# Kernel optimization log

Hardware: AMD Instinct MI355X
Metric: run time of the kernel (lower is better)

The kernel has to match this reference:

```python
import jax, jax.numpy as jnp
import numpy as np

DEPTH_SCALES = 4  # matches init_kwargs
REDUCTION = 16    # CBAM-style MLP reduction ratio


def setup_inputs() -> dict:
    key = jax.random.key(0)
    k0, k1, k2 = jax.random.split(key, 3)
    N, C, H, W = 32, 512, 64, 64
    D, r = DEPTH_SCALES, REDUCTION
    x = jax.random.normal(k0, (N, C, H, W), dtype=jnp.float32)
    # shared 2-layer gate MLP: C -> C//r -> C*D
    W1 = jax.random.normal(k1, (C, C // r), dtype=jnp.float32) * 0.05
    b1 = jnp.zeros((C // r,), dtype=jnp.float32)
    W2 = jax.random.normal(k2, (C // r, C * D), dtype=jnp.float32) * 0.05
    b2 = jnp.zeros((C * D,), dtype=jnp.float32)
    return {"x": x, "W1": W1, "b1": b1, "W2": W2, "b2": b2}


def reference(x, W1, b1, W2, b2):
    N, C, H, W = x.shape
    D = DEPTH_SCALES
    block = C // D  # block_size

    # ExpandedChannelGate (CBAM-style): avg+max spatial pooling through a
    # shared MLP, summed, sigmoid -> attention [N, C, D]
    avg_pool = jnp.mean(x, axis=(2, 3))  # [N, C]
    max_pool = jnp.max(x, axis=(2, 3))   # [N, C]

    def mlp(p):
        return jax.nn.relu(p @ W1 + b1) @ W2 + b2  # [N, C*D]

    attn = jax.nn.sigmoid(mlp(avg_pool) + mlp(max_pool))  # [N, C*D]
    attn = attn.reshape(N, C, D).transpose(0, 2, 1)       # [N, D, C]

    # topk over the channel axis per (sample, scale); lax.top_k sorts
    # descending like torch.topk
    _, idx = jax.lax.top_k(attn, block)  # [N, D, block]

    # Original concatenates scale-i selections along channel dim, i.e.
    # channel order = [scale0 topk..., scale1 topk..., ...].
    idx_flat = idx.reshape(N, D * block)  # [N, C]

    # single vectorized gather replaces the nested index_select loops
    out = jax.vmap(lambda xi, ii: xi[ii])(x, idx_flat)  # [N, D*block, H, W]
    return out
```

## Files before the change

### kernel.cpp

```cpp
#include <hip/hip_runtime.h>
#include <hip/hip_bf16.h>
#include <math.h>

#define N_ 32
#define C_ 512
#define HW_ 4096
#define D_ 4
#define RHID_ 32
#define BLOCK_ 128
#define C2_ 2048

__global__ __launch_bounds__(256) void pool_kernel(
    const float* __restrict__ x, float* __restrict__ avg_out,
    float* __restrict__ max_out) {
  const int b = blockIdx.x;
  const float4* src = (const float4*)(x + (size_t)b * HW_);
  const int t = threadIdx.x;

  double dsum = 0.0;
  float mx = -INFINITY;
#pragma unroll
  for (int i = 0; i < 4; ++i) {
    float4 v = src[t + i * 256];
    dsum += (double)v.x + (double)v.y + (double)v.z + (double)v.w;
    mx = fmaxf(mx, fmaxf(fmaxf(v.x, v.y), fmaxf(v.z, v.w)));
  }
#pragma unroll
  for (int off = 32; off > 0; off >>= 1) {
    dsum += __shfl_down(dsum, off);
    mx = fmaxf(mx, __shfl_down(mx, off));
  }
  __shared__ double s_sum[4];
  __shared__ float s_max[4];
  const int wave = t >> 6;
  if ((t & 63) == 0) { s_sum[wave] = dsum; s_max[wave] = mx; }
  __syncthreads();
  if (t == 0) {
    double tot = s_sum[0] + s_sum[1] + s_sum[2] + s_sum[3];
    float m = fmaxf(fmaxf(s_max[0], s_max[1]), fmaxf(s_max[2], s_max[3]));
    avg_out[b] = (float)(tot * (1.0 / (double)HW_));
    max_out[b] = m;
  }
}

__global__ __launch_bounds__(256) void mlp_topk_kernel(
    const float* __restrict__ avg, const float* __restrict__ mx,
    const float* __restrict__ W1, const float* __restrict__ b1,
    const float* __restrict__ W2, const float* __restrict__ b2,
    int* __restrict__ idx_out) {
  const int n = blockIdx.x >> 2;
  const int d = blockIdx.x & 3;
  const int t = threadIdx.x;

  __shared__ float s_avg[C_];
  __shared__ float s_mx[C_];
  __shared__ double s_h[RHID_];
  __shared__ unsigned long long s_key[C_];

#pragma unroll
  for (int i = 0; i < 2; ++i) {
    int c = t + i * 256;
    s_avg[c] = avg[n * C_ + c];
    s_mx[c] = mx[n * C_ + c];
  }
  __syncthreads();

  if (t < RHID_) {
    double acc_a = (double)b1[t];
    double acc_m = acc_a;
    for (int c = 0; c < C_; ++c) {
      double w = (double)W1[c * RHID_ + t];
      acc_a += (double)s_avg[c] * w;
      acc_m += (double)s_mx[c] * w;
    }
    s_h[t] = (acc_a > 0.0 ? acc_a : 0.0) + (acc_m > 0.0 ? acc_m : 0.0);
  }
  __syncthreads();

  for (int c = t; c < C_; c += 256) {
    const int col = c * D_ + d;
    double acc = 2.0 * (double)b2[col];
#pragma unroll
    for (int j = 0; j < RHID_; ++j)
      acc += s_h[j] * (double)W2[j * C2_ + col];
    float f = (float)acc;
    unsigned u = __float_as_uint(f);
    u = (u & 0x80000000u) ? ~u : (u | 0x80000000u);
    s_key[c] = ((unsigned long long)u << 32) | (unsigned)(C_ - 1 - c);
  }
  __syncthreads();

  for (int kk = 2; kk <= C_; kk <<= 1) {
    for (int jj = kk >> 1; jj > 0; jj >>= 1) {
#pragma unroll
      for (int r = 0; r < 2; ++r) {
        int i = t + r * 256;
        int ixj = i ^ jj;
        if (ixj > i) {
          bool ddd = ((i & kk) != 0);
          unsigned long long a = s_key[i], b = s_key[ixj];
          if ((a > b) == ddd) { s_key[i] = b; s_key[ixj] = a; }
        }
      }
      __syncthreads();
    }
  }

  if (t < BLOCK_) {
    int c = (C_ - 1) - (int)(s_key[t] & 0xFFFFFFFFu);
    idx_out[(n * D_ + d) * BLOCK_ + t] = c;
  }
}

__global__ __launch_bounds__(256) void gather_kernel(
    const float* __restrict__ x, const int* __restrict__ idx,
    float* __restrict__ out) {
  const int b = blockIdx.x;
  const int n = b >> 9;
  const int c = idx[b];
  const float4* src = (const float4*)(x + ((size_t)(n * C_ + c)) * HW_);
  float4* dst = (float4*)(out + (size_t)b * HW_);
  const int t = threadIdx.x;
#pragma unroll
  for (int i = 0; i < 4; ++i) dst[t + i * 256] = src[t + i * 256];
}

extern "C" void kernel_launch(void* const* d_in, const int* in_sizes, int n_in,
                              void* d_out, int out_size, void* d_ws, size_t ws_size,
                              hipStream_t stream) {
  const float* x  = (const float*)d_in[0];
  const float* W1 = (const float*)d_in[1];
  const float* b1 = (const float*)d_in[2];
  const float* W2 = (const float*)d_in[3];
  const float* b2 = (const float*)d_in[4];
  float* out = (float*)d_out;

  float* ws_avg = (float*)d_ws;
  float* ws_max = ws_avg + N_ * C_;
  int* ws_idx = (int*)(ws_max + N_ * C_);

  pool_kernel<<<N_ * C_, 256, 0, stream>>>(x, ws_avg, ws_max);
  mlp_topk_kernel<<<N_ * D_, 256, 0, stream>>>(ws_avg, ws_max, W1, b1, W2, b2,
                                               ws_idx);
  gather_kernel<<<N_ * C_, 256, 0, stream>>>(x, ws_idx, out);
}
```

Measured before the change: 544.7 us.

## Assign one wavefront per channel in pool/gather and parallelize first MLP layer

Pool and gather kernels now map each 64-lane wavefront to one channel plane, with four planes per block. This drops the shared-memory cross-wave reduction and __syncthreads in pooling, and gives each thread more loads in flight. The gather uses nontemporal stores so the written output does not evict x from cache. The first MLP layer is split across all 256 threads into 8 partial sums reduced in shared memory, replacing a 32-thread serial loop over 512 channels.

```diff
diff --git a/kernel.cpp b/kernel.cpp
--- a/kernel.cpp
+++ b/kernel.cpp
@@ -1,5 +1,4 @@
 #include <hip/hip_runtime.h>
-#include <hip/hip_bf16.h>
 #include <math.h>
 
 #define N_ 32
@@ -10,18 +9,20 @@
 #define BLOCK_ 128
 #define C2_ 2048
 
+typedef float vfloat4 __attribute__((ext_vector_type(4)));
+
 __global__ __launch_bounds__(256) void pool_kernel(
     const float* __restrict__ x, float* __restrict__ avg_out,
     float* __restrict__ max_out) {
-  const int b = blockIdx.x;
-  const float4* src = (const float4*)(x + (size_t)b * HW_);
-  const int t = threadIdx.x;
+  const int p = (blockIdx.x << 2) + (threadIdx.x >> 6);
+  const int lane = threadIdx.x & 63;
+  const vfloat4* src = (const vfloat4*)(x + (size_t)p * HW_);
 
   double dsum = 0.0;
   float mx = -INFINITY;
 #pragma unroll
-  for (int i = 0; i < 4; ++i) {
-    float4 v = src[t + i * 256];
+  for (int i = 0; i < 16; ++i) {
+    vfloat4 v = src[lane + (i << 6)];
     dsum += (double)v.x + (double)v.y + (double)v.z + (double)v.w;
     mx = fmaxf(mx, fmaxf(fmaxf(v.x, v.y), fmaxf(v.z, v.w)));
   }
@@ -30,16 +31,9 @@
     dsum += __shfl_down(dsum, off);
     mx = fmaxf(mx, __shfl_down(mx, off));
   }
-  __shared__ double s_sum[4];
-  __shared__ float s_max[4];
-  const int wave = t >> 6;
-  if ((t & 63) == 0) { s_sum[wave] = dsum; s_max[wave] = mx; }
-  __syncthreads();
-  if (t == 0) {
-    double tot = s_sum[0] + s_sum[1] + s_sum[2] + s_sum[3];
-    float m = fmaxf(fmaxf(s_max[0], s_max[1]), fmaxf(s_max[2], s_max[3]));
-    avg_out[b] = (float)(tot * (1.0 / (double)HW_));
-    max_out[b] = m;
+  if (lane == 0) {
+    avg_out[p] = (float)(dsum * (1.0 / (double)HW_));
+    max_out[p] = mx;
   }
 }
 
@@ -54,6 +48,8 @@
 
   __shared__ float s_avg[C_];
   __shared__ float s_mx[C_];
+  __shared__ double s_pa[8][RHID_];
+  __shared__ double s_pm[8][RHID_];
   __shared__ double s_h[RHID_];
   __shared__ unsigned long long s_key[C_];
 
@@ -65,15 +61,30 @@
   }
   __syncthreads();
 
+  {
+    const int j = t & 31;
+    const int g = t >> 5;
+    double pa = 0.0, pm = 0.0;
+#pragma unroll 4
+    for (int i = 0; i < 64; ++i) {
+      const int c = (g << 6) + i;
+      const double w = (double)W1[c * RHID_ + j];
+      pa += (double)s_avg[c] * w;
+      pm += (double)s_mx[c] * w;
+    }
+    s_pa[g][j] = pa;
+    s_pm[g][j] = pm;
+  }
+  __syncthreads();
   if (t < RHID_) {
-    double acc_a = (double)b1[t];
-    double acc_m = acc_a;
-    for (int c = 0; c < C_; ++c) {
-      double w = (double)W1[c * RHID_ + t];
-      acc_a += (double)s_avg[c] * w;
-      acc_m += (double)s_mx[c] * w;
+    double a = (double)b1[t];
+    double m = a;
+#pragma unroll
+    for (int g = 0; g < 8; ++g) {
+      a += s_pa[g][t];
+      m += s_pm[g][t];
     }
-    s_h[t] = (acc_a > 0.0 ? acc_a : 0.0) + (acc_m > 0.0 ? acc_m : 0.0);
+    s_h[t] = (a > 0.0 ? a : 0.0) + (m > 0.0 ? m : 0.0);
   }
   __syncthreads();
 
@@ -115,14 +126,17 @@
 __global__ __launch_bounds__(256) void gather_kernel(
     const float* __restrict__ x, const int* __restrict__ idx,
     float* __restrict__ out) {
-  const int b = blockIdx.x;
-  const int n = b >> 9;
-  const int c = idx[b];
-  const float4* src = (const float4*)(x + ((size_t)(n * C_ + c)) * HW_);
-  float4* dst = (float4*)(out + (size_t)b * HW_);
-  const int t = threadIdx.x;
+  const int p = (blockIdx.x << 2) + (threadIdx.x >> 6);
+  const int lane = threadIdx.x & 63;
+  const int n = p >> 9;
+  const int c = idx[p];
+  const vfloat4* src = (const vfloat4*)(x + ((size_t)(n * C_ + c)) * HW_);
+  vfloat4* dst = (vfloat4*)(out + (size_t)p * HW_);
 #pragma unroll
-  for (int i = 0; i < 4; ++i) dst[t + i * 256] = src[t + i * 256];
+  for (int i = 0; i < 16; ++i) {
+    vfloat4 v = src[lane + (i << 6)];
+    __builtin_nontemporal_store(v, &dst[lane + (i << 6)]);
+  }
 }
 
 extern "C" void kernel_launch(void* const* d_in, const int* in_sizes, int n_in,
@@ -139,8 +153,8 @@
   float* ws_max = ws_avg + N_ * C_;
   int* ws_idx = (int*)(ws_max + N_ * C_);
 
-  pool_kernel<<<N_ * C_, 256, 0, stream>>>(x, ws_avg, ws_max);
+  pool_kernel<<<(N_ * C_) / 4, 256, 0, stream>>>(x, ws_avg, ws_max);
   mlp_topk_kernel<<<N_ * D_, 256, 0, stream>>>(ws_avg, ws_max, W1, b1, W2, b2,
                                                ws_idx);
-  gather_kernel<<<N_ * C_, 256, 0, stream>>>(x, ws_idx, out);
+  gather_kernel<<<(N_ * C_) / 4, 256, 0, stream>>>(x, ws_idx, out);
 }
```

Measured after the change: 518.7 us. 1.05x faster.
